# Performance work log

Measured on AMD Instinct MI355X. Metric: run time of the kernel, lower is better.

The kernel has to match this reference:

```python
import jax, jax.numpy as jnp
import numpy as np

NEG_INF = -jnp.inf

def _sage_conv(x_src, x_dst, src, dst, Wl, bl, Wr, aggr, num_nodes):
    # messages = source features gathered along edges  [E, d]
    msgs = x_src[src]
    if aggr == 'mean':
        s = jax.ops.segment_sum(msgs, dst, num_segments=num_nodes)
        cnt = jax.ops.segment_sum(jnp.ones((src.shape[0],), x_src.dtype), dst, num_segments=num_nodes)
        agg = s / jnp.maximum(cnt, 1.0)[:, None]
    else:  # max; isolated targets -> 0 (PyG scatter-max fill)
        m = jax.ops.segment_max(msgs, dst, num_segments=num_nodes)
        agg = jnp.where(jnp.isfinite(m), m, 0.0)
    return agg @ Wl.T + bl + x_dst @ Wr.T

def setup_inputs() -> dict:
    key = jax.random.key(0)
    ks = jax.random.split(key, 12)
    N, E, D, H, C, L = 40000, 640000, 128, 128, 64, 2
    sc = 0.05
    return {
        'x': jax.random.normal(ks[0], (N, D), jnp.float32),
        'edge_index0': jax.random.randint(ks[1], (2, E), 0, N, jnp.int64),
        'edge_index1': jax.random.randint(ks[2], (2, E), 0, N, jnp.int64),
        'Wl_mean': jax.random.normal(ks[3], (L, H, D), jnp.float32) * sc,
        'bl_mean': jax.random.normal(ks[4], (L, H), jnp.float32) * sc,
        'Wr_mean': jax.random.normal(ks[5], (L, H, D), jnp.float32) * sc,
        'Wl_max': jax.random.normal(ks[6], (L, H, D), jnp.float32) * sc,
        'bl_max': jax.random.normal(ks[7], (L, H), jnp.float32) * sc,
        'Wr_max': jax.random.normal(ks[8], (L, H, D), jnp.float32) * sc,
        'post_W': jax.random.normal(ks[9], (C, 2 * L * H), jnp.float32) * sc,
        'post_b': jax.random.normal(ks[10], (C,), jnp.float32) * sc,
    }

def reference(x, edge_index0, edge_index1, Wl_mean, bl_mean, Wr_mean, Wl_max, bl_max, Wr_max, post_W, post_b):
    N = x.shape[0]
    edge_sets = [edge_index0, edge_index1]
    L = len(edge_sets)
    h = x
    all_layers = []
    for i, ei in enumerate(edge_sets):
        src, dst = ei[0], ei[1]
        x_mean = _sage_conv(h, h, src, dst, Wl_mean[i], bl_mean[i], Wr_mean[i], 'mean', N)
        x_max = _sage_conv(h, h, src, dst, Wl_max[i], bl_max[i], Wr_max[i], 'max', N)
        all_layers.append(x_mean)
        all_layers.append(x_max)
        if i != L - 1:
            h = jax.nn.relu(h)  # note: original never replaces x with conv output
    x_final = jnp.concatenate(all_layers, axis=1) @ post_W.T + post_b
    return jax.nn.log_softmax(x_final, axis=-1)
```

## Files before the change

### kernel.cpp

```cpp
#include <hip/hip_runtime.h>
#include <cstdint>
#include <cstddef>

constexpr int FD = 128;
constexpr int CC = 64;
constexpr int KTOT = 768;
constexpr int CAP = 48;
constexpr int EPT = 4;

typedef __attribute__((ext_vector_type(8))) short short8;
typedef __attribute__((ext_vector_type(4))) float f32x4;

__device__ __forceinline__ float bf2f(unsigned u16) {
  union { unsigned u; float f; } v; v.u = u16 << 16; return v.f;
}
__device__ __forceinline__ unsigned f2bf(float f) {
  union { float f; unsigned u; } v; v.f = f;
  return (v.u + 0x7FFFu + ((v.u >> 16) & 1u)) >> 16;
}
__device__ __forceinline__ unsigned pack2(float a, float b) {
  return f2bf(a) | (f2bf(b) << 16);
}
__device__ __forceinline__ unsigned relu_pk(unsigned v) {
  unsigned m = ((v >> 15) & 0x10001u) * 0xFFFFu;
  return v & ~m;
}

__global__ void init_kernel(const float* __restrict__ x, uint4* __restrict__ xbf4,
                            int n8, int* __restrict__ cnt, int ncnt) {
  int t = blockIdx.x * blockDim.x + threadIdx.x;
  if (t < ncnt) cnt[t] = 0;
  if (t >= n8) return;
  float4 a = *(const float4*)(x + (size_t)t * 8);
  float4 b = *(const float4*)(x + (size_t)t * 8 + 4);
  uint4 q;
  q.x = pack2(a.x, a.y); q.y = pack2(a.z, a.w);
  q.z = pack2(b.x, b.y); q.w = pack2(b.z, b.w);
  xbf4[t] = q;
}

__global__ void precompute_kernel(
    const float* __restrict__ Wl_mean, const float* __restrict__ bl_mean,
    const float* __restrict__ Wr_mean, const float* __restrict__ Wl_max,
    const float* __restrict__ bl_max,  const float* __restrict__ Wr_max,
    const float* __restrict__ postW,   const float* __restrict__ postb,
    unsigned short* __restrict__ Mbf, float* __restrict__ cb)
{
  int t = blockIdx.x * blockDim.x + threadIdx.x;
  if (t >= KTOT * CC) return;
  int c  = t & (CC - 1);
  int k  = t >> 6;
  int blk = k >> 7;
  int kk  = k & 127;
  const float* pw = postW + (size_t)c * 512;
  float acc = 0.f;
  if (blk < 4) {
    const float* W;
    if (blk == 0)      W = Wl_mean;
    else if (blk == 1) W = Wl_max;
    else if (blk == 2) W = Wl_mean + 128 * 128;
    else               W = Wl_max + 128 * 128;
    const float* p = pw + blk * 128;
    #pragma unroll 8
    for (int h = 0; h < 128; ++h) acc += p[h] * W[h * 128 + kk];
  } else if (blk == 4) {
    #pragma unroll 8
    for (int h = 0; h < 128; ++h)
      acc += pw[h] * Wr_mean[h * 128 + kk] + pw[128 + h] * Wr_max[h * 128 + kk];
  } else {
    const float* Wm = Wr_mean + 128 * 128;
    const float* Wx = Wr_max + 128 * 128;
    #pragma unroll 8
    for (int h = 0; h < 128; ++h)
      acc += pw[256 + h] * Wm[h * 128 + kk] + pw[384 + h] * Wx[h * 128 + kk];
  }
  Mbf[(size_t)c * KTOT + k] = (unsigned short)f2bf(acc);

  if (t < CC) {
    const float* pwc = postW + (size_t)t * 512;
    float b = postb[t];
    for (int h = 0; h < 128; ++h) {
      b += bl_mean[h]        * pwc[h]
         + bl_max[h]         * pwc[128 + h]
         + bl_mean[128 + h]  * pwc[256 + h]
         + bl_max[128 + h]   * pwc[384 + h];
    }
    cb[t] = b;
  }
}

__global__ __launch_bounds__(256) void build_kernel(
    const int* __restrict__ e0, int E0,
    const int* __restrict__ e1, int E1,
    int* __restrict__ cnt, unsigned short* __restrict__ csrf, int N)
{
  int t = blockIdx.x * blockDim.x + threadIdx.x;
  const int nt0 = (E0 + EPT - 1) / EPT;
  const int nt1 = (E1 + EPT - 1) / EPT;
  if (t >= nt0 + nt1) return;
  const int twoN = 2 * N;
  const int* e; int E; int cb2; int ti;
  if (t < nt0) { e = e0; E = E0; cb2 = 0; ti = t; }
  else         { e = e1; E = E1; cb2 = N; ti = t - nt0; }
  const int i0 = ti * EPT;

  if (i0 + EPT <= E) {
    int4 s4 = *(const int4*)(e + i0);
    int4 d4 = *(const int4*)(e + E + i0);
    int s[EPT] = {s4.x, s4.y, s4.z, s4.w};
    int d[EPT] = {d4.x, d4.y, d4.z, d4.w};
    int p[EPT];
    #pragma unroll
    for (int u = 0; u < EPT; ++u) p[u] = atomicAdd(&cnt[cb2 + d[u]], 1);
    #pragma unroll
    for (int u = 0; u < EPT; ++u)
      if (p[u] < CAP) csrf[(size_t)p[u] * twoN + cb2 + d[u]] = (unsigned short)s[u];
  } else {
    const int n = E - i0;
    for (int u = 0; u < n; ++u) {
      int ss = e[i0 + u], dd = e[E + i0 + u];
      int pp = atomicAdd(&cnt[cb2 + dd], 1);
      if (pp < CAP) csrf[(size_t)pp * twoN + cb2 + dd] = (unsigned short)ss;
    }
  }
}

__global__ __launch_bounds__(256) void agg_kernel(
    const unsigned* __restrict__ xbf, const int* __restrict__ cnt,
    const unsigned short* __restrict__ csrf, unsigned* __restrict__ aggbf, int N)
{
  int gw = (blockIdx.x * 256 + threadIdx.x) >> 6;
  int lane = threadIdx.x & 63;
  if (gw >= 2 * N) return;
  const int twoN = 2 * N;
  const int layer = (gw >= N) ? 1 : 0;
  const int node = gw - layer * N;
  const int deg = min(cnt[gw], CAP);
  const int half = lane >> 5;
  const int hl = lane & 31;
  const float lo = layer ? 0.f : -INFINITY;

  const int n0 = (deg + 1) >> 1;
  const int cbeg = half ? n0 : 0;
  const int ce = half ? deg : n0;

  float s0 = 0.f, s1 = 0.f, s2 = 0.f, s3 = 0.f;
  float m0 = -INFINITY, m1 = -INFINITY, m2 = -INFINITY, m3 = -INFINITY;

  for (int c = cbeg; c < ce; c += 8) {
    int idx[8];
    bool val[8];
    #pragma unroll
    for (int u = 0; u < 8; ++u) {
      int cc = c + u;
      val[u] = cc < ce;
      idx[u] = (int)csrf[(size_t)(val[u] ? cc : (ce - 1)) * twoN + gw];
    }
    uint2 g[8];
    #pragma unroll
    for (int u = 0; u < 8; ++u)
      g[u] = *(const uint2*)(xbf + (size_t)idx[u] * 64 + hl * 2);
    #pragma unroll
    for (int u = 0; u < 8; ++u) {
      float a0 = fmaxf(bf2f(g[u].x & 0xffffu), lo);
      float a1 = fmaxf(bf2f(g[u].x >> 16), lo);
      float a2 = fmaxf(bf2f(g[u].y & 0xffffu), lo);
      float a3 = fmaxf(bf2f(g[u].y >> 16), lo);
      s0 += val[u] ? a0 : 0.f;  s1 += val[u] ? a1 : 0.f;
      s2 += val[u] ? a2 : 0.f;  s3 += val[u] ? a3 : 0.f;
      m0 = fmaxf(m0, val[u] ? a0 : -INFINITY);
      m1 = fmaxf(m1, val[u] ? a1 : -INFINITY);
      m2 = fmaxf(m2, val[u] ? a2 : -INFINITY);
      m3 = fmaxf(m3, val[u] ? a3 : -INFINITY);
    }
  }

  s0 += __shfl_xor(s0, 32); s1 += __shfl_xor(s1, 32);
  s2 += __shfl_xor(s2, 32); s3 += __shfl_xor(s3, 32);
  m0 = fmaxf(m0, __shfl_xor(m0, 32)); m1 = fmaxf(m1, __shfl_xor(m1, 32));
  m2 = fmaxf(m2, __shfl_xor(m2, 32)); m3 = fmaxf(m3, __shfl_xor(m3, 32));

  if (half == 0) {
    float inv = 1.f / (float)(deg > 0 ? deg : 1);
    if (deg == 0) { m0 = 0.f; m1 = 0.f; m2 = 0.f; m3 = 0.f; }
    unsigned* am = aggbf + (size_t)(layer * 2)     * N * 64;
    unsigned* ax = aggbf + (size_t)(layer * 2 + 1) * N * 64;
    size_t o = (size_t)node * 64 + hl * 2;
    *(uint2*)(am + o) = make_uint2(pack2(s0 * inv, s1 * inv), pack2(s2 * inv, s3 * inv));
    *(uint2*)(ax + o) = make_uint2(pack2(m0, m1), pack2(m2, m3));
  }
}

__global__ __launch_bounds__(256) void gemm_kernel(
    const unsigned* __restrict__ aggbf, const unsigned* __restrict__ xbf,
    const unsigned short* __restrict__ Mbf, const float* __restrict__ cb,
    float* __restrict__ out, int N)
{
  const int tid = threadIdx.x;
  const int w = tid >> 6, l = tid & 63;
  const int l15 = l & 15, lg = l >> 4;
  const int rowb = blockIdx.x * 128 + w * 32;
  const int r0 = rowb + l15, r1 = r0 + 16;
  const size_t a0r = (size_t)min(r0, N - 1) * 64;
  const size_t a1r = (size_t)min(r1, N - 1) * 64;
  const int kg = lg * 8;
  const size_t N64 = (size_t)N * 64;

  f32x4 acc[2][4];
  #pragma unroll
  for (int i = 0; i < 2; ++i)
    #pragma unroll
    for (int j = 0; j < 4; ++j) acc[i][j] = (f32x4){0.f, 0.f, 0.f, 0.f};

  #pragma unroll
  for (int b6 = 0; b6 < 6; ++b6) {
    const unsigned* Ap = (b6 < 4) ? (aggbf + (size_t)b6 * N64) : xbf;
    #pragma unroll
    for (int ss = 0; ss < 4; ++ss) {
      const int k0 = b6 * 128 + ss * 32;
      const int ko = (ss * 32 + kg) >> 1;
      uint4 ua = *(const uint4*)(Ap + a0r + ko);
      uint4 ub = *(const uint4*)(Ap + a1r + ko);
      if (b6 == 5) {
        ua.x = relu_pk(ua.x); ua.y = relu_pk(ua.y);
        ua.z = relu_pk(ua.z); ua.w = relu_pk(ua.w);
        ub.x = relu_pk(ub.x); ub.y = relu_pk(ub.y);
        ub.z = relu_pk(ub.z); ub.w = relu_pk(ub.w);
      }
      short8 af0 = __builtin_bit_cast(short8, ua);
      short8 af1 = __builtin_bit_cast(short8, ub);
      #pragma unroll
      for (int fc = 0; fc < 4; ++fc) {
        const int c = fc * 16 + l15;
        uint4 qb = *(const uint4*)(Mbf + (size_t)c * KTOT + k0 + kg);
        short8 bf = __builtin_bit_cast(short8, qb);
        acc[0][fc] = __builtin_amdgcn_mfma_f32_16x16x32_bf16(af0, bf, acc[0][fc], 0, 0, 0);
        acc[1][fc] = __builtin_amdgcn_mfma_f32_16x16x32_bf16(af1, bf, acc[1][fc], 0, 0, 0);
      }
    }
  }

  float bias[4];
  #pragma unroll
  for (int fc = 0; fc < 4; ++fc) bias[fc] = cb[fc * 16 + l15];

  #pragma unroll
  for (int fr = 0; fr < 2; ++fr) {
    #pragma unroll
    for (int i = 0; i < 4; ++i) {
      int row = rowb + fr * 16 + lg * 4 + i;
      float z0 = acc[fr][0][i] + bias[0];
      float z1 = acc[fr][1][i] + bias[1];
      float z2 = acc[fr][2][i] + bias[2];
      float z3 = acc[fr][3][i] + bias[3];
      float m = fmaxf(fmaxf(z0, z1), fmaxf(z2, z3));
      #pragma unroll
      for (int o = 1; o < 16; o <<= 1) m = fmaxf(m, __shfl_xor(m, o));
      float s = expf(z0 - m) + expf(z1 - m) + expf(z2 - m) + expf(z3 - m);
      #pragma unroll
      for (int o = 1; o < 16; o <<= 1) s += __shfl_xor(s, o);
      float lse = m + logf(s);
      if (row < N) {
        size_t ob = (size_t)row * CC + l15;
        out[ob]      = z0 - lse;
        out[ob + 16] = z1 - lse;
        out[ob + 32] = z2 - lse;
        out[ob + 48] = z3 - lse;
      }
    }
  }
}

extern "C" void kernel_launch(void* const* d_in, const int* in_sizes, int n_in,
                              void* d_out, int out_size, void* d_ws, size_t ws_size,
                              hipStream_t stream)
{
  const float* x       = (const float*)d_in[0];
  const int*   e0      = (const int*)d_in[1];
  const int*   e1      = (const int*)d_in[2];
  const float* Wl_mean = (const float*)d_in[3];
  const float* bl_mean = (const float*)d_in[4];
  const float* Wr_mean = (const float*)d_in[5];
  const float* Wl_max  = (const float*)d_in[6];
  const float* bl_max  = (const float*)d_in[7];
  const float* Wr_max  = (const float*)d_in[8];
  const float* postW   = (const float*)d_in[9];
  const float* postb   = (const float*)d_in[10];
  float* out = (float*)d_out;

  const int N  = in_sizes[0] / FD;
  const int E0 = in_sizes[1] / 2;
  const int E1 = in_sizes[2] / 2;

  char* ws = (char*)d_ws;
  size_t off = 0;
  auto alloc = [&](size_t bytes) -> void* {
    void* p = ws + off;
    off = (off + bytes + 255) & ~(size_t)255;
    return p;
  };
  unsigned short* Mbf  = (unsigned short*)alloc((size_t)KTOT * CC * 2);
  float*          cbv  = (float*)alloc(CC * 4);
  int*            cnt  = (int*)alloc((size_t)2 * N * 4);
  unsigned short* csrf = (unsigned short*)alloc((size_t)2 * N * CAP * 2);
  unsigned*       xbf  = (unsigned*)alloc((size_t)N * 64 * 4);
  unsigned*       aggbf= (unsigned*)alloc((size_t)4 * N * 64 * 4);
  (void)ws_size; (void)n_in; (void)out_size;

  const int n8 = N * 16;
  init_kernel<<<dim3((n8 + 255) / 256), dim3(256), 0, stream>>>(
      x, (uint4*)xbf, n8, cnt, 2 * N);

  precompute_kernel<<<dim3((KTOT * CC + 255) / 256), dim3(256), 0, stream>>>(
      Wl_mean, bl_mean, Wr_mean, Wl_max, bl_max, Wr_max, postW, postb, Mbf, cbv);

  const int nthr = (E0 + EPT - 1) / EPT + (E1 + EPT - 1) / EPT;
  build_kernel<<<dim3((nthr + 255) / 256), dim3(256), 0, stream>>>(
      e0, E0, e1, E1, cnt, csrf, N);

  const int aggBlocks = (2 * N * 64 + 255) / 256;
  agg_kernel<<<dim3(aggBlocks), dim3(256), 0, stream>>>(xbf, cnt, csrf, aggbf, N);

  gemm_kernel<<<dim3((N + 127) / 128), dim3(256), 0, stream>>>(
      aggbf, xbf, Mbf, cbv, out, N);
}
```

Measured before the change: 277.6 us.

## Partition CSR build by destination range, merge init kernels, shrink GEMM tile

The CSR build now splits destination nodes into 8 ranges. Each block scans a 4096-edge stripe and inserts only the edges whose target falls in its range, so atomics and scattered writes stay within a smaller region, likely chosen for cache locality on the XCDs. The init and precompute kernels are merged into one grid-stride kernel to save a launch. The GEMM drops from 32 to 16 rows per wave, which doubles the block count and lowers register use. The trade-off is that every edge's destination is read 8 times in the build.

New measurement: 275.3 us. No clear change (-0.8%).

```diff
diff --git a/kernel.cpp b/kernel.cpp
--- a/kernel.cpp
+++ b/kernel.cpp
@@ -6,7 +6,7 @@
 constexpr int CC = 64;
 constexpr int KTOT = 768;
 constexpr int CAP = 48;
-constexpr int EPT = 4;
+constexpr int SS = 4096;
 
 typedef __attribute__((ext_vector_type(8))) short short8;
 typedef __attribute__((ext_vector_type(4))) float f32x4;
@@ -26,116 +26,117 @@
   return v & ~m;
 }
 
-__global__ void init_kernel(const float* __restrict__ x, uint4* __restrict__ xbf4,
-                            int n8, int* __restrict__ cnt, int ncnt) {
-  int t = blockIdx.x * blockDim.x + threadIdx.x;
-  if (t < ncnt) cnt[t] = 0;
-  if (t >= n8) return;
-  float4 a = *(const float4*)(x + (size_t)t * 8);
-  float4 b = *(const float4*)(x + (size_t)t * 8 + 4);
-  uint4 q;
-  q.x = pack2(a.x, a.y); q.y = pack2(a.z, a.w);
-  q.z = pack2(b.x, b.y); q.w = pack2(b.z, b.w);
-  xbf4[t] = q;
-}
-
-__global__ void precompute_kernel(
+__global__ __launch_bounds__(256) void initpre_kernel(
+    const float* __restrict__ x, uint4* __restrict__ xbf4, int n8,
+    int* __restrict__ cnt, int ncnt,
     const float* __restrict__ Wl_mean, const float* __restrict__ bl_mean,
     const float* __restrict__ Wr_mean, const float* __restrict__ Wl_max,
     const float* __restrict__ bl_max,  const float* __restrict__ Wr_max,
     const float* __restrict__ postW,   const float* __restrict__ postb,
     unsigned short* __restrict__ Mbf, float* __restrict__ cb)
 {
-  int t = blockIdx.x * blockDim.x + threadIdx.x;
-  if (t >= KTOT * CC) return;
-  int c  = t & (CC - 1);
-  int k  = t >> 6;
-  int blk = k >> 7;
-  int kk  = k & 127;
-  const float* pw = postW + (size_t)c * 512;
-  float acc = 0.f;
-  if (blk < 4) {
-    const float* W;
-    if (blk == 0)      W = Wl_mean;
-    else if (blk == 1) W = Wl_max;
-    else if (blk == 2) W = Wl_mean + 128 * 128;
-    else               W = Wl_max + 128 * 128;
-    const float* p = pw + blk * 128;
-    #pragma unroll 8
-    for (int h = 0; h < 128; ++h) acc += p[h] * W[h * 128 + kk];
-  } else if (blk == 4) {
-    #pragma unroll 8
-    for (int h = 0; h < 128; ++h)
-      acc += pw[h] * Wr_mean[h * 128 + kk] + pw[128 + h] * Wr_max[h * 128 + kk];
-  } else {
-    const float* Wm = Wr_mean + 128 * 128;
-    const float* Wx = Wr_max + 128 * 128;
-    #pragma unroll 8
-    for (int h = 0; h < 128; ++h)
-      acc += pw[256 + h] * Wm[h * 128 + kk] + pw[384 + h] * Wx[h * 128 + kk];
-  }
-  Mbf[(size_t)c * KTOT + k] = (unsigned short)f2bf(acc);
-
-  if (t < CC) {
-    const float* pwc = postW + (size_t)t * 512;
-    float b = postb[t];
-    for (int h = 0; h < 128; ++h) {
-      b += bl_mean[h]        * pwc[h]
-         + bl_max[h]         * pwc[128 + h]
-         + bl_mean[128 + h]  * pwc[256 + h]
-         + bl_max[128 + h]   * pwc[384 + h];
-    }
-    cb[t] = b;
+  const int gtid = blockIdx.x * 256 + threadIdx.x;
+  const int gsz = gridDim.x * 256;
+
+  for (int t = gtid; t < ncnt; t += gsz) cnt[t] = 0;
+
+  for (int t = gtid; t < n8; t += gsz) {
+    float4 a = *(const float4*)(x + (size_t)t * 8);
+    float4 b = *(const float4*)(x + (size_t)t * 8 + 4);
+    uint4 q;
+    q.x = pack2(a.x, a.y); q.y = pack2(a.z, a.w);
+    q.z = pack2(b.x, b.y); q.w = pack2(b.z, b.w);
+    xbf4[t] = q;
+  }
+
+  for (int t = gtid; t < KTOT * CC; t += gsz) {
+    int c  = t & (CC - 1);
+    int k  = t >> 6;
+    int blk = k >> 7;
+    int kk  = k & 127;
+    const float* pw = postW + (size_t)c * 512;
+    float acc = 0.f;
+    if (blk < 4) {
+      const float* W;
+      if (blk == 0)      W = Wl_mean;
+      else if (blk == 1) W = Wl_max;
+      else if (blk == 2) W = Wl_mean + 128 * 128;
+      else               W = Wl_max + 128 * 128;
+      const float* pp = pw + blk * 128;
+      #pragma unroll 8
+      for (int h = 0; h < 128; ++h) acc += pp[h] * W[h * 128 + kk];
+    } else if (blk == 4) {
+      #pragma unroll 8
+      for (int h = 0; h < 128; ++h)
+        acc += pw[h] * Wr_mean[h * 128 + kk] + pw[128 + h] * Wr_max[h * 128 + kk];
+    } else {
+      const float* Wm = Wr_mean + 128 * 128;
+      const float* Wx = Wr_max + 128 * 128;
+      #pragma unroll 8
+      for (int h = 0; h < 128; ++h)
+        acc += pw[256 + h] * Wm[h * 128 + kk] + pw[384 + h] * Wx[h * 128 + kk];
+    }
+    Mbf[(size_t)c * KTOT + k] = (unsigned short)f2bf(acc);
+
+    if (t < CC) {
+      const float* pwc = postW + (size_t)t * 512;
+      float b = postb[t];
+      for (int h = 0; h < 128; ++h) {
+        b += bl_mean[h]        * pwc[h]
+           + bl_max[h]         * pwc[128 + h]
+           + bl_mean[128 + h]  * pwc[256 + h]
+           + bl_max[128 + h]   * pwc[384 + h];
+      }
+      cb[t] = b;
+    }
   }
 }
 
 __global__ __launch_bounds__(256) void build_kernel(
     const int* __restrict__ e0, int E0,
     const int* __restrict__ e1, int E1,
-    int* __restrict__ cnt, unsigned short* __restrict__ csrf, int N)
-{
-  int t = blockIdx.x * blockDim.x + threadIdx.x;
-  const int nt0 = (E0 + EPT - 1) / EPT;
-  const int nt1 = (E1 + EPT - 1) / EPT;
-  if (t >= nt0 + nt1) return;
-  const int twoN = 2 * N;
-  const int* e; int E; int cb2; int ti;
-  if (t < nt0) { e = e0; E = E0; cb2 = 0; ti = t; }
-  else         { e = e1; E = E1; cb2 = N; ti = t - nt0; }
-  const int i0 = ti * EPT;
-
-  if (i0 + EPT <= E) {
-    int4 s4 = *(const int4*)(e + i0);
-    int4 d4 = *(const int4*)(e + E + i0);
-    int s[EPT] = {s4.x, s4.y, s4.z, s4.w};
-    int d[EPT] = {d4.x, d4.y, d4.z, d4.w};
-    int p[EPT];
-    #pragma unroll
-    for (int u = 0; u < EPT; ++u) p[u] = atomicAdd(&cnt[cb2 + d[u]], 1);
-    #pragma unroll
-    for (int u = 0; u < EPT; ++u)
-      if (p[u] < CAP) csrf[(size_t)p[u] * twoN + cb2 + d[u]] = (unsigned short)s[u];
-  } else {
-    const int n = E - i0;
-    for (int u = 0; u < n; ++u) {
-      int ss = e[i0 + u], dd = e[E + i0 + u];
-      int pp = atomicAdd(&cnt[cb2 + dd], 1);
-      if (pp < CAP) csrf[(size_t)pp * twoN + cb2 + dd] = (unsigned short)ss;
+    int* __restrict__ cnt, unsigned short* __restrict__ csrf, int N, int NC)
+{
+  const int b = blockIdx.x;
+  const int c = b & 7;
+  const int t = b >> 3;
+  const int nst0 = (E0 + SS - 1) / SS;
+  const int* e; int E; int s; int stripe;
+  if (t < nst0) { e = e0; E = E0; s = 0; stripe = t; }
+  else          { e = e1; E = E1; s = 1; stripe = t - nst0; }
+  const int lo = c * NC;
+  const int hi = min(N, lo + NC);
+  const int i0 = stripe * SS;
+  const int i1 = min(E, i0 + SS);
+  int* mycnt = cnt + (size_t)(s * 8 + c) * NC;
+  unsigned short* mycsr = csrf + (size_t)(s * 8 + c) * NC * CAP;
+
+  for (int i = i0 + threadIdx.x; i < i1; i += 256) {
+    int d = e[E + i];
+    if (d >= lo && d < hi) {
+      int srcv = e[i];
+      int n_ = d - lo;
+      int pos = atomicAdd(&mycnt[n_], 1);
+      if (pos < CAP) mycsr[(size_t)pos * NC + n_] = (unsigned short)srcv;
     }
   }
 }
 
 __global__ __launch_bounds__(256) void agg_kernel(
     const unsigned* __restrict__ xbf, const int* __restrict__ cnt,
-    const unsigned short* __restrict__ csrf, unsigned* __restrict__ aggbf, int N)
+    const unsigned short* __restrict__ csrf, unsigned* __restrict__ aggbf,
+    int N, int NC)
 {
   int gw = (blockIdx.x * 256 + threadIdx.x) >> 6;
   int lane = threadIdx.x & 63;
   if (gw >= 2 * N) return;
-  const int twoN = 2 * N;
   const int layer = (gw >= N) ? 1 : 0;
   const int node = gw - layer * N;
-  const int deg = min(cnt[gw], CAP);
+  const int cls = node / NC;
+  const int n_ = node - cls * NC;
+  const int reg = layer * 8 + cls;
+  const int deg = min(cnt[(size_t)reg * NC + n_], CAP);
+  const unsigned short* cs = csrf + (size_t)reg * NC * CAP + n_;
   const int half = lane >> 5;
   const int hl = lane & 31;
   const float lo = layer ? 0.f : -INFINITY;
@@ -154,7 +155,7 @@
     for (int u = 0; u < 8; ++u) {
       int cc = c + u;
       val[u] = cc < ce;
-      idx[u] = (int)csrf[(size_t)(val[u] ? cc : (ce - 1)) * twoN + gw];
+      idx[u] = (int)cs[(size_t)(val[u] ? cc : (ce - 1)) * NC];
     }
     uint2 g[8];
     #pragma unroll
@@ -199,18 +200,15 @@
   const int tid = threadIdx.x;
   const int w = tid >> 6, l = tid & 63;
   const int l15 = l & 15, lg = l >> 4;
-  const int rowb = blockIdx.x * 128 + w * 32;
-  const int r0 = rowb + l15, r1 = r0 + 16;
-  const size_t a0r = (size_t)min(r0, N - 1) * 64;
-  const size_t a1r = (size_t)min(r1, N - 1) * 64;
   const int kg = lg * 8;
   const size_t N64 = (size_t)N * 64;
-
-  f32x4 acc[2][4];
+  const int rowb = blockIdx.x * 64 + w * 16;
+  const int r0 = rowb + l15;
+  const size_t a0r = (size_t)min(r0, N - 1) * 64;
+
+  f32x4 acc[4];
   #pragma unroll
-  for (int i = 0; i < 2; ++i)
-    #pragma unroll
-    for (int j = 0; j < 4; ++j) acc[i][j] = (f32x4){0.f, 0.f, 0.f, 0.f};
+  for (int j = 0; j < 4; ++j) acc[j] = (f32x4){0.f, 0.f, 0.f, 0.f};
 
   #pragma unroll
   for (int b6 = 0; b6 < 6; ++b6) {
@@ -220,22 +218,17 @@
       const int k0 = b6 * 128 + ss * 32;
       const int ko = (ss * 32 + kg) >> 1;
       uint4 ua = *(const uint4*)(Ap + a0r + ko);
-      uint4 ub = *(const uint4*)(Ap + a1r + ko);
       if (b6 == 5) {
         ua.x = relu_pk(ua.x); ua.y = relu_pk(ua.y);
         ua.z = relu_pk(ua.z); ua.w = relu_pk(ua.w);
-        ub.x = relu_pk(ub.x); ub.y = relu_pk(ub.y);
-        ub.z = relu_pk(ub.z); ub.w = relu_pk(ub.w);
       }
-      short8 af0 = __builtin_bit_cast(short8, ua);
-      short8 af1 = __builtin_bit_cast(short8, ub);
+      short8 af = __builtin_bit_cast(short8, ua);
       #pragma unroll
       for (int fc = 0; fc < 4; ++fc) {
         const int c = fc * 16 + l15;
         uint4 qb = *(const uint4*)(Mbf + (size_t)c * KTOT + k0 + kg);
         short8 bf = __builtin_bit_cast(short8, qb);
-        acc[0][fc] = __builtin_amdgcn_mfma_f32_16x16x32_bf16(af0, bf, acc[0][fc], 0, 0, 0);
-        acc[1][fc] = __builtin_amdgcn_mfma_f32_16x16x32_bf16(af1, bf, acc[1][fc], 0, 0, 0);
+        acc[fc] = __builtin_amdgcn_mfma_f32_16x16x32_bf16(af, bf, acc[fc], 0, 0, 0);
       }
     }
   }
@@ -245,28 +238,25 @@
   for (int fc = 0; fc < 4; ++fc) bias[fc] = cb[fc * 16 + l15];
 
   #pragma unroll
-  for (int fr = 0; fr < 2; ++fr) {
-    #pragma unroll
-    for (int i = 0; i < 4; ++i) {
-      int row = rowb + fr * 16 + lg * 4 + i;
-      float z0 = acc[fr][0][i] + bias[0];
-      float z1 = acc[fr][1][i] + bias[1];
-      float z2 = acc[fr][2][i] + bias[2];
-      float z3 = acc[fr][3][i] + bias[3];
-      float m = fmaxf(fmaxf(z0, z1), fmaxf(z2, z3));
-      #pragma unroll
-      for (int o = 1; o < 16; o <<= 1) m = fmaxf(m, __shfl_xor(m, o));
-      float s = expf(z0 - m) + expf(z1 - m) + expf(z2 - m) + expf(z3 - m);
-      #pragma unroll
-      for (int o = 1; o < 16; o <<= 1) s += __shfl_xor(s, o);
-      float lse = m + logf(s);
-      if (row < N) {
-        size_t ob = (size_t)row * CC + l15;
-        out[ob]      = z0 - lse;
-        out[ob + 16] = z1 - lse;
-        out[ob + 32] = z2 - lse;
-        out[ob + 48] = z3 - lse;
-      }
+  for (int i = 0; i < 4; ++i) {
+    int row = rowb + lg * 4 + i;
+    float z0 = acc[0][i] + bias[0];
+    float z1 = acc[1][i] + bias[1];
+    float z2 = acc[2][i] + bias[2];
+    float z3 = acc[3][i] + bias[3];
+    float m = fmaxf(fmaxf(z0, z1), fmaxf(z2, z3));
+    #pragma unroll
+    for (int o = 1; o < 16; o <<= 1) m = fmaxf(m, __shfl_xor(m, o));
+    float s = expf(z0 - m) + expf(z1 - m) + expf(z2 - m) + expf(z3 - m);
+    #pragma unroll
+    for (int o = 1; o < 16; o <<= 1) s += __shfl_xor(s, o);
+    float lse = m + logf(s);
+    if (row < N) {
+      size_t ob = (size_t)row * CC + l15;
+      out[ob]      = z0 - lse;
+      out[ob + 16] = z1 - lse;
+      out[ob + 32] = z2 - lse;
+      out[ob + 48] = z3 - lse;
     }
   }
 }
@@ -291,6 +281,7 @@
   const int N  = in_sizes[0] / FD;
   const int E0 = in_sizes[1] / 2;
   const int E1 = in_sizes[2] / 2;
+  const int NC = (N + 7) / 8;
 
   char* ws = (char*)d_ws;
   size_t off = 0;
@@ -301,26 +292,24 @@
   };
   unsigned short* Mbf  = (unsigned short*)alloc((size_t)KTOT * CC * 2);
   float*          cbv  = (float*)alloc(CC * 4);
-  int*            cnt  = (int*)alloc((size_t)2 * N * 4);
-  unsigned short* csrf = (unsigned short*)alloc((size_t)2 * N * CAP * 2);
+  int*            cnt  = (int*)alloc((size_t)16 * NC * 4);
+  unsigned short* csrf = (unsigned short*)alloc((size_t)16 * NC * CAP * 2);
   unsigned*       xbf  = (unsigned*)alloc((size_t)N * 64 * 4);
   unsigned*       aggbf= (unsigned*)alloc((size_t)4 * N * 64 * 4);
   (void)ws_size; (void)n_in; (void)out_size;
 
   const int n8 = N * 16;
-  init_kernel<<<dim3((n8 + 255) / 256), dim3(256), 0, stream>>>(
-      x, (uint4*)xbf, n8, cnt, 2 * N);
-
-  precompute_kernel<<<dim3((KTOT * CC + 255) / 256), dim3(256), 0, stream>>>(
+  initpre_kernel<<<dim3(1024), dim3(256), 0, stream>>>(
+      x, (uint4*)xbf, n8, cnt, 16 * NC,
       Wl_mean, bl_mean, Wr_mean, Wl_max, bl_max, Wr_max, postW, postb, Mbf, cbv);
 
-  const int nthr = (E0 + EPT - 1) / EPT + (E1 + EPT - 1) / EPT;
-  build_kernel<<<dim3((nthr + 255) / 256), dim3(256), 0, stream>>>(
-      e0, E0, e1, E1, cnt, csrf, N);
+  const int nst = (E0 + SS - 1) / SS + (E1 + SS - 1) / SS;
+  build_kernel<<<dim3(8 * nst), dim3(256), 0, stream>>>(
+      e0, E0, e1, E1, cnt, csrf, N, NC);
 
   const int aggBlocks = (2 * N * 64 + 255) / 256;
-  agg_kernel<<<dim3(aggBlocks), dim3(256), 0, stream>>>(xbf, cnt, csrf, aggbf, N);
-
-  gemm_kernel<<<dim3((N + 127) / 128), dim3(256), 0, stream>>>(
+  agg_kernel<<<dim3(aggBlocks), dim3(256), 0, stream>>>(xbf, cnt, csrf, aggbf, N, NC);
+
+  gemm_kernel<<<dim3((N + 63) / 64), dim3(256), 0, stream>>>(
       aggbf, xbf, Mbf, cbv, out, N);
 }
```
